# Performance work log

Hardware: AMD Instinct MI355X
Metric: run time of the kernel (lower is better)

## Reference

```python
import jax, jax.numpy as jnp
import numpy as np

I, H, O, L = 128, 1024, 128, 2

def _linear_init(key, out_f, in_f, bias):
    b = 1.0 / np.sqrt(in_f)
    kw, kb = jax.random.split(key)
    W = jax.random.uniform(kw, (out_f, in_f), jnp.float32, -b, b)
    if bias:
        return W, jax.random.uniform(kb, (out_f,), jnp.float32, -b, b)
    return W, None

def setup_inputs() -> dict:
    key = jax.random.key(0)
    ks = jax.random.split(key, 32)
    inp = {
        'x': jax.random.normal(ks[0], (32, 512, I), jnp.float32),
        'h0': jnp.zeros((32, L, H), jnp.float32),
    }
    ki = 1
    in_dim = I
    for l in range(L):
        Wxz, _ = _linear_init(ks[ki], H, in_dim, False); ki += 1
        Whz, bz = _linear_init(ks[ki], H, H, True); ki += 1
        Wxr, _ = _linear_init(ks[ki], H, in_dim, False); ki += 1
        Whr, br = _linear_init(ks[ki], H, H, True); ki += 1
        Wxg, _ = _linear_init(ks[ki], H, in_dim, False); ki += 1
        Whg, bg = _linear_init(ks[ki], H, H, True); ki += 1
        inp.update({f'Wxz{l}': Wxz, f'Whz{l}': Whz, f'bz{l}': bz,
                    f'Wxr{l}': Wxr, f'Whr{l}': Whr, f'br{l}': br,
                    f'Wxg{l}': Wxg, f'Whg{l}': Whg, f'bg{l}': bg})
        in_dim = H
    Wy, by = _linear_init(ks[ki], O, H, True)
    inp['Wy'] = Wy
    inp['by'] = by
    return inp

def _gru_layer(x_seq, h0, Wxz, Whz, bz, Wxr, Whr, br, Wxg, Whg, bg):
    # Precompute all input projections as big GEMMs (B,S,H)
    xz = jnp.einsum('bsi,hi->bsh', x_seq, Wxz)
    xr = jnp.einsum('bsi,hi->bsh', x_seq, Wxr)
    xg = jnp.einsum('bsi,hi->bsh', x_seq, Wxg)
    def step(h, gates):
        gz, gr, gg = gates
        z = jax.nn.sigmoid(gz + h @ Whz.T + bz)
        r = jax.nn.sigmoid(gr + h @ Whr.T + br)
        g = jnp.tanh(gg + (r * h) @ Whg.T + bg)
        h_new = z * h + (1.0 - z) * g
        return h_new, h_new
    # scan over time: (S,B,H)
    hT, hs = jax.lax.scan(step, h0, (xz.transpose(1, 0, 2), xr.transpose(1, 0, 2), xg.transpose(1, 0, 2)))
    return hs.transpose(1, 0, 2), hT

def reference(x, h0,
              Wxz0, Whz0, bz0, Wxr0, Whr0, br0, Wxg0, Whg0, bg0,
              Wxz1, Whz1, bz1, Wxr1, Whr1, br1, Wxg1, Whg1, bg1,
              Wy, by):
    layers = [
        (Wxz0, Whz0, bz0, Wxr0, Whr0, br0, Wxg0, Whg0, bg0),
        (Wxz1, Whz1, bz1, Wxr1, Whr1, br1, Wxg1, Whg1, bg1),
    ]
    seq = x
    finals = []
    for l, p in enumerate(layers):
        seq, hT = _gru_layer(seq, h0[:, l, :], *p)
        finals.append(hT)
    y = jnp.einsum('bsh,oh->bso', seq, Wy) + by  # (B,S,O)
    hidden = jnp.stack(finals, axis=1)  # (B,L,H)
    return y, hidden
```

## Files before the change

### kernel.cpp

```cpp
#include <hip/hip_runtime.h>

typedef unsigned short u16;
typedef unsigned int u32;
typedef unsigned long long u64;
typedef __bf16 bf16x8 __attribute__((ext_vector_type(8)));
typedef float f32x4 __attribute__((ext_vector_type(4)));

union FU { f32x4 f; bf16x8 h; };

__device__ __forceinline__ u16 f2b(float f) {
  unsigned u = __float_as_uint(f);
  return (u16)((u + 0x7fffu + ((u >> 16) & 1u)) >> 16);
}

__device__ __forceinline__ void st_b16_llc(u16* p, u16 v) {
  __hip_atomic_store(p, v, __ATOMIC_RELAXED, __HIP_MEMORY_SCOPE_AGENT);
}

__device__ __forceinline__ u32 ld_dword_cc(const u32* p) {
  u32 v;
  asm volatile("global_load_dword %0, %1, off sc0 sc1\n\ts_waitcnt vmcnt(0)"
               : "=v"(v) : "v"(p) : "memory");
  return v;
}

#define ISSUE8CC(D, P)                                                       \
  asm volatile(                                                              \
      "global_load_dwordx4 %0, %8, off sc0 sc1\n\t"                          \
      "global_load_dwordx4 %1, %8, off offset:64 sc0 sc1\n\t"                \
      "global_load_dwordx4 %2, %8, off offset:128 sc0 sc1\n\t"               \
      "global_load_dwordx4 %3, %8, off offset:192 sc0 sc1\n\t"               \
      "global_load_dwordx4 %4, %8, off offset:256 sc0 sc1\n\t"               \
      "global_load_dwordx4 %5, %8, off offset:320 sc0 sc1\n\t"               \
      "global_load_dwordx4 %6, %8, off offset:384 sc0 sc1\n\t"               \
      "global_load_dwordx4 %7, %8, off offset:448 sc0 sc1"                   \
      : "=&v"((D)[0].f), "=&v"((D)[1].f), "=&v"((D)[2].f), "=&v"((D)[3].f),  \
        "=&v"((D)[4].f), "=&v"((D)[5].f), "=&v"((D)[6].f), "=&v"((D)[7].f)   \
      : "v"(P) : "memory")

#define ISSUE4C(D, P)                                                        \
  asm volatile(                                                              \
      "global_load_dwordx4 %0, %4, off\n\t"                                  \
      "global_load_dwordx4 %1, %4, off offset:64\n\t"                        \
      "global_load_dwordx4 %2, %4, off offset:128\n\t"                       \
      "global_load_dwordx4 %3, %4, off offset:192"                           \
      : "=&v"((D)[0].f), "=&v"((D)[1].f), "=&v"((D)[2].f), "=&v"((D)[3].f)   \
      : "v"(P) : "memory")

#define WAITV(N)                                                             \
  do {                                                                       \
    asm volatile("s_waitcnt vmcnt(" #N ")" ::: "memory");                    \
    __builtin_amdgcn_sched_barrier(0);                                       \
  } while (0)

#define MFMA8ZR(ACC, BUF, KSB)                                               \
  do {                                                                       \
    _Pragma("unroll") for (int j_ = 0; j_ < 8; ++j_)                         \
        ACC = __builtin_amdgcn_mfma_f32_16x16x32_bf16(                       \
            (BUF)[j_].h,                                                     \
            *(const bf16x8*)&zr_frag[(KSB + j_) * 512 + lane * 8],           \
            ACC, 0, 0, 0);                                                   \
  } while (0)
#define MFMA8G(ACC, BUF, KSB)                                                \
  do {                                                                       \
    _Pragma("unroll") for (int j_ = 0; j_ < 8; ++j_)                         \
        ACC = __builtin_amdgcn_mfma_f32_16x16x32_bf16(                       \
            (BUF)[j_].h,                                                     \
            *(const bf16x8*)&g_frag[(KSB + j_) * 256 + boff],                \
            ACC, 0, 0, 0);                                                   \
  } while (0)

__global__ void cast_f32_bf16(const float* __restrict__ in, u16* __restrict__ out, int n) {
  int i = blockIdx.x * 256 + threadIdx.x;
  if (i < n) out[i] = f2b(in[i]);
}

__device__ __forceinline__ void wg_bar(u32* __restrict__ slots, u32 ep,
                                       int bid, int tid, int lane, int w) {
  __syncthreads();
  const int g = bid >> 5;
  u32* gslots = slots + 256;
  if (tid == 0)
    __hip_atomic_store(&slots[g * 32 + (bid & 31)], ep,
                       __ATOMIC_RELAXED, __HIP_MEMORY_SCOPE_AGENT);
  if (w == 0) {
    if ((bid & 31) == 0) {
      const u32* grp = slots + g * 32;
      for (;;) {
        u32 v = ep;
        if (lane < 32) v = ld_dword_cc(&grp[lane]);
        if (__all(v >= ep)) break;
        __builtin_amdgcn_s_sleep(1);
      }
      if (lane == 0)
        __hip_atomic_store(&gslots[g], ep,
                           __ATOMIC_RELAXED, __HIP_MEMORY_SCOPE_AGENT);
    }
    for (;;) {
      u32 v = ld_dword_cc(&gslots[lane & 7]);
      if (__all(v >= ep)) break;
      __builtin_amdgcn_s_sleep(1);
    }
  }
  __syncthreads();
}

__global__ __launch_bounds__(256) void gemm_bt(
    const u16* __restrict__ A, const u16* __restrict__ B,
    int M, int N, int K,
    const float* __restrict__ bias, float* __restrict__ Cf)
{
  __shared__ u16 a_sm[128 * 32];
  __shared__ u16 b_sm[128 * 32];
  const int tid = threadIdx.x;
  const int lane = tid & 63;
  const int wid = tid >> 6;
  const int wm = wid >> 1, wn = wid & 1;
  const int m0 = blockIdx.x * 128, n0 = blockIdx.y * 128;
  const int q = lane >> 4, l15 = lane & 15, l3 = lane & 3;

  f32x4 acc[4][4];
  #pragma unroll
  for (int i = 0; i < 4; ++i)
    #pragma unroll
    for (int j = 0; j < 4; ++j) acc[i][j] = (f32x4){0.f, 0.f, 0.f, 0.f};

  for (int kk = 0; kk < K; kk += 32) {
    __syncthreads();
    #pragma unroll
    for (int p = 0; p < 2; ++p) {
      int idx = p * 256 + tid;
      int r = idx >> 2, cch = idx & 3;
      *(uint4*)&a_sm[r * 32 + ((cch ^ (r & 3)) * 8)] =
          *(const uint4*)&A[(size_t)(m0 + r) * K + kk + cch * 8];
      *(uint4*)&b_sm[r * 32 + ((cch ^ (r & 3)) * 8)] =
          *(const uint4*)&B[(size_t)(n0 + r) * K + kk + cch * 8];
    }
    __syncthreads();
    bf16x8 af[4], bfr[4];
    #pragma unroll
    for (int s = 0; s < 4; ++s) {
      int ra = wm * 64 + s * 16 + l15;
      af[s] = *(const bf16x8*)&a_sm[ra * 32 + ((q ^ l3) * 8)];
      int rb = wn * 64 + s * 16 + l15;
      bfr[s] = *(const bf16x8*)&b_sm[rb * 32 + ((q ^ l3) * 8)];
    }
    #pragma unroll
    for (int si = 0; si < 4; ++si)
      #pragma unroll
      for (int sj = 0; sj < 4; ++sj)
        acc[si][sj] = __builtin_amdgcn_mfma_f32_16x16x32_bf16(af[si], bfr[sj], acc[si][sj], 0, 0, 0);
  }

  #pragma unroll
  for (int si = 0; si < 4; ++si)
    #pragma unroll
    for (int sj = 0; sj < 4; ++sj)
      #pragma unroll
      for (int e = 0; e < 4; ++e) {
        int m = m0 + wm * 64 + si * 16 + q * 4 + e;
        int n = n0 + wn * 64 + sj * 16 + l15;
        Cf[(size_t)m * N + n] = acc[si][sj][e] + (bias ? bias[n] : 0.f);
      }
}

__global__ __launch_bounds__(128, 1) void gru_pipe(
    const u16* __restrict__ Wh0, const u16* __restrict__ Wx0,
    const u16* __restrict__ Wh1, const u16* __restrict__ Wx1,
    const float* __restrict__ bz0, const float* __restrict__ br0, const float* __restrict__ bg0,
    const float* __restrict__ bz1, const float* __restrict__ br1, const float* __restrict__ bg1,
    const u16* __restrict__ xb,
    const float* __restrict__ h0p,
    u16* __restrict__ h0buf,
    u16* __restrict__ hb1,
    u16* __restrict__ rh0b, u16* __restrict__ rh1b,
    u16* __restrict__ seq1,
    float* __restrict__ hid,
    u32* __restrict__ slots)
{
  __shared__ u16 zr_frag[64 * 512];
  __shared__ u16 g_frag[64 * 256];

  const int tid = threadIdx.x;
  const int lane = tid & 63;
  const int w = tid >> 6;
  const int bid = blockIdx.x;
  const bool Lyr1 = bid >= 128;
  const int nb = (bid & 127) * 8;
  const int q = lane >> 4, c15 = lane & 15, nl = c15 & 7;
  const int n_own = nb + nl;
  const bool isz = c15 < 8;
  const int brow = w * 16 + c15;
  const int boff = (q * 8 + nl) * 8;
  const int aoff = brow * 1024 + q * 8;
  const int KS = Lyr1 ? 64 : 36;
  const int IN = Lyr1 ? 1024 : 128;
  const u16* Wh = Lyr1 ? Wh1 : Wh0;
  const u16* Wx = Lyr1 ? Wx1 : Wx0;
  const size_t WXG = (size_t)1024 * IN;

  for (int cidx = tid; cidx < KS * 64; cidx += 128) {
    int ks = cidx >> 6, l = cidx & 63;
    int lq = l >> 4, lc = l & 15;
    int row = nb + (lc & 7), gate = (lc < 8) ? 0 : 1;
    int k0 = ks * 32 + lq * 8;
    const u16* src = (k0 < 1024)
        ? Wh + (size_t)gate * 1048576 + (size_t)row * 1024 + k0
        : Wx + (size_t)gate * WXG + (size_t)row * IN + (k0 - 1024);
    *(uint4*)&zr_frag[cidx * 8] = *(const uint4*)src;
  }
  for (int gidx = tid; gidx < KS * 32; gidx += 128) {
    int ks = gidx >> 5, s = gidx & 31;
    int lq = s >> 3, r8 = s & 7;
    int row = nb + r8, k0 = ks * 32 + lq * 8;
    const u16* src = (k0 < 1024)
        ? Wh + (size_t)2 * 1048576 + (size_t)row * 1024 + k0
        : Wx + (size_t)2 * WXG + (size_t)row * IN + (k0 - 1024);
    *(uint4*)&g_frag[gidx * 8] = *(const uint4*)src;
  }

  const float bias1 = isz ? (Lyr1 ? bz1 : bz0)[n_own] : (Lyr1 ? br1 : br0)[n_own];
  const float bias2 = (Lyr1 ? bg1 : bg0)[n_own];

  float hreg[4], zreg[4] = {0.f, 0.f, 0.f, 0.f};
  #pragma unroll
  for (int e = 0; e < 4; ++e) {
    int b = w * 16 + q * 4 + e;
    float v = h0p[b * 2048 + (Lyr1 ? 1024 : 0) + n_own];
    hreg[e] = v;
    if (isz)
      st_b16_llc((Lyr1 ? hb1 : h0buf + 32768) + b * 1024 + n_own, f2b(v));
  }
  wg_bar(slots, 1, bid, tid, lane, w);

  FU xfu[4];
  FU sA[8], sB[8], sC[8];

  for (int p = 0; p < 1026; ++p) {
    const int t = p >> 1, ph = p & 1;
    if (!Lyr1) {
      if (t < 512) {
        f32x4 a0 = {0.f,0.f,0.f,0.f}, a1 = {0.f,0.f,0.f,0.f};
        if (ph == 0) {
          const u16* hp = h0buf + ((t - 1) & 1) * 32768 + aoff;
          const u16* xp = xb + ((size_t)brow * 512 + t) * 128 + q * 8;
          ISSUE4C(xfu, xp);
          ISSUE8CC(sA, hp);
          ISSUE8CC(sB, hp + 256);
          ISSUE8CC(sC, hp + 512);
          WAITV(16); MFMA8ZR(a0, sA, 0);
          ISSUE8CC(sA, hp + 768);
          WAITV(16); MFMA8ZR(a0, sB, 8);
          WAITV(8);  MFMA8ZR(a0, sC, 16);
          WAITV(0);  MFMA8ZR(a0, sA, 24);
          #pragma unroll
          for (int j = 0; j < 4; ++j)
            a1 = __builtin_amdgcn_mfma_f32_16x16x32_bf16(
                xfu[j].h, *(const bf16x8*)&zr_frag[(32 + j) * 512 + lane * 8], a1, 0, 0, 0);
          float hsh[4];
          #pragma unroll
          for (int e = 0; e < 4; ++e) hsh[e] = __shfl_xor(hreg[e], 8);
          #pragma unroll
          for (int e = 0; e < 4; ++e) {
            float pre = a0[e] + a1[e] + bias1;
            float s = 1.f / (1.f + __expf(-pre));
            if (isz) zreg[e] = s;
            else st_b16_llc(&rh0b[(w * 16 + q * 4 + e) * 1024 + n_own], f2b(s * hsh[e]));
          }
        } else {
          const u16* rp = rh0b + aoff;
          ISSUE8CC(sA, rp);
          ISSUE8CC(sB, rp + 256);
          ISSUE8CC(sC, rp + 512);
          WAITV(16); MFMA8G(a0, sA, 0);
          ISSUE8CC(sA, rp + 768);
          WAITV(16); MFMA8G(a0, sB, 8);
          WAITV(8);  MFMA8G(a0, sC, 16);
          WAITV(0);  MFMA8G(a0, sA, 24);
          #pragma unroll
          for (int j = 0; j < 4; ++j)
            a1 = __builtin_amdgcn_mfma_f32_16x16x32_bf16(
                xfu[j].h, *(const bf16x8*)&g_frag[(32 + j) * 256 + boff], a1, 0, 0, 0);
          if (isz) {
            u16* hout = h0buf + (t & 1) * 32768;
            #pragma unroll
            for (int e = 0; e < 4; ++e) {
              int b = w * 16 + q * 4 + e;
              float pre = a0[e] + a1[e] + bias2;
              float ex = __expf(2.f * pre);
              float gv = 1.f - 2.f / (ex + 1.f);
              float hn = zreg[e] * hreg[e] + (1.f - zreg[e]) * gv;
              hreg[e] = hn;
              st_b16_llc(&hout[b * 1024 + n_own], f2b(hn));
              if (t == 511) hid[b * 2048 + n_own] = hn;
            }
          }
        }
      }
    } else {
      if (t >= 1) {
        const int s = t - 1;
        f32x4 a0 = {0.f,0.f,0.f,0.f}, a1 = {0.f,0.f,0.f,0.f};
        const u16* hp = h0buf + (s & 1) * 32768 + aoff;
        if (ph == 0) {
          const u16* hb = hb1 + aoff;
          ISSUE8CC(sA, hb);
          ISSUE8CC(sB, hb + 256);
          ISSUE8CC(sC, hb + 512);
          WAITV(16); MFMA8ZR(a0, sA, 0);  ISSUE8CC(sA, hb + 768);
          WAITV(16); MFMA8ZR(a0, sB, 8);  ISSUE8CC(sB, hp);
          WAITV(16); MFMA8ZR(a0, sC, 16); ISSUE8CC(sC, hp + 256);
          WAITV(16); MFMA8ZR(a0, sA, 24); ISSUE8CC(sA, hp + 512);
          WAITV(16); MFMA8ZR(a1, sB, 32); ISSUE8CC(sB, hp + 768);
          WAITV(16); MFMA8ZR(a1, sC, 40);
          WAITV(8);  MFMA8ZR(a1, sA, 48);
          WAITV(0);  MFMA8ZR(a1, sB, 56);
          float hsh[4];
          #pragma unroll
          for (int e = 0; e < 4; ++e) hsh[e] = __shfl_xor(hreg[e], 8);
          #pragma unroll
          for (int e = 0; e < 4; ++e) {
            float pre = a0[e] + a1[e] + bias1;
            float sg = 1.f / (1.f + __expf(-pre));
            if (isz) zreg[e] = sg;
            else st_b16_llc(&rh1b[(w * 16 + q * 4 + e) * 1024 + n_own], f2b(sg * hsh[e]));
          }
        } else {
          const u16* rp = rh1b + aoff;
          ISSUE8CC(sA, rp);
          ISSUE8CC(sB, rp + 256);
          ISSUE8CC(sC, rp + 512);
          WAITV(16); MFMA8G(a0, sA, 0);  ISSUE8CC(sA, rp + 768);
          WAITV(16); MFMA8G(a0, sB, 8);  ISSUE8CC(sB, hp);
          WAITV(16); MFMA8G(a0, sC, 16); ISSUE8CC(sC, hp + 256);
          WAITV(16); MFMA8G(a0, sA, 24); ISSUE8CC(sA, hp + 512);
          WAITV(16); MFMA8G(a1, sB, 32); ISSUE8CC(sB, hp + 768);
          WAITV(16); MFMA8G(a1, sC, 40);
          WAITV(8);  MFMA8G(a1, sA, 48);
          WAITV(0);  MFMA8G(a1, sB, 56);
          if (isz) {
            #pragma unroll
            for (int e = 0; e < 4; ++e) {
              int b = w * 16 + q * 4 + e;
              float pre = a0[e] + a1[e] + bias2;
              float ex = __expf(2.f * pre);
              float gv = 1.f - 2.f / (ex + 1.f);
              float hn = zreg[e] * hreg[e] + (1.f - zreg[e]) * gv;
              hreg[e] = hn;
              u16 hnb = f2b(hn);
              st_b16_llc(&hb1[b * 1024 + n_own], hnb);
              seq1[((size_t)b * 512 + s) * 1024 + n_own] = hnb;
              if (s == 511) hid[1024 + b * 2048 + n_own] = hn;
            }
          }
        }
      }
    }
    if (p < 1025) wg_bar(slots, (u32)(p + 2), bid, tid, lane, w);
  }
}

extern "C" void kernel_launch(void* const* d_in, const int* in_sizes, int n_in,
                              void* d_out, int out_size, void* d_ws, size_t ws_size,
                              hipStream_t stream) {
  (void)in_sizes; (void)n_in; (void)out_size; (void)ws_size;
  char* ws = (char*)d_ws;
  const size_t MB = 1024ull * 1024ull;
  u16* seq1 = (u16*)(ws + 0);
  u16* xb   = (u16*)(ws + 32 * MB);
  u16* Wh0  = (u16*)(ws + 36 * MB);
  u16* Wh1  = (u16*)(ws + 42 * MB);
  u16* Wx0  = (u16*)(ws + 48 * MB);
  u16* Wx1  = (u16*)(ws + 49 * MB);
  u16* Wyb  = (u16*)(ws + 55 * MB);
  u16* h0buf = (u16*)(ws + 56 * MB);
  u16* hb1  = (u16*)(ws + 56 * MB + 128 * 1024);
  u16* rh0b = (u16*)(ws + 56 * MB + 192 * 1024);
  u16* rh1b = (u16*)(ws + 56 * MB + 256 * 1024);
  u32* slots = (u32*)(ws + 56 * MB + 320 * 1024);

  hipMemsetAsync(slots, 0, 2048, stream);

  auto cast = [&](const void* in, u16* out, int n) {
    cast_f32_bf16<<<(n + 255) / 256, 256, 0, stream>>>((const float*)in, out, n);
  };
  cast(d_in[0], xb, 2097152);
  cast(d_in[3],  Wh0 + 0,       1048576);
  cast(d_in[6],  Wh0 + 1048576, 1048576);
  cast(d_in[9],  Wh0 + 2097152, 1048576);
  cast(d_in[12], Wh1 + 0,       1048576);
  cast(d_in[15], Wh1 + 1048576, 1048576);
  cast(d_in[18], Wh1 + 2097152, 1048576);
  cast(d_in[2],  Wx0 + 0,      131072);
  cast(d_in[5],  Wx0 + 131072, 131072);
  cast(d_in[8],  Wx0 + 262144, 131072);
  cast(d_in[11], Wx1 + 0,       1048576);
  cast(d_in[14], Wx1 + 1048576, 1048576);
  cast(d_in[17], Wx1 + 2097152, 1048576);
  cast(d_in[20], Wyb, 131072);

  float* y_out = (float*)d_out;
  float* hid = y_out + 2097152;

  gru_pipe<<<256, dim3(128), 0, stream>>>(
      Wh0, Wx0, Wh1, Wx1,
      (const float*)d_in[4],  (const float*)d_in[7],  (const float*)d_in[10],
      (const float*)d_in[13], (const float*)d_in[16], (const float*)d_in[19],
      xb, (const float*)d_in[1],
      h0buf, hb1, rh0b, rh1b, seq1, hid, slots);

  gemm_bt<<<dim3(128, 1), dim3(256), 0, stream>>>(
      seq1, Wyb, 16384, 128, 1024, (const float*)d_in[21], y_out);
}
```

Before: 6.572 ms.

## Replace hierarchical grid barrier with per-wave dependency flags and aggregator wave

Removes the two-level workgroup grid barrier run every pipeline phase. Each compute wave now publishes its own progress counter, and a dedicated third wave in block 0 reduces the counters per dependency group and broadcasts them to replicated flag slots. Each wave waits only on the groups it actually depends on (its own layer, and the other layer with a phase-dependent target) instead of on all blocks. This cuts barrier latency and __syncthreads stalls on the recurrent critical path, at the cost of an extra polling wave, a more fragile ordering protocol, and reliance on the aggregator's polling latency.

```diff
diff --git a/kernel.cpp b/kernel.cpp
--- a/kernel.cpp
+++ b/kernel.cpp
@@ -15,6 +15,10 @@
 
 __device__ __forceinline__ void st_b16_llc(u16* p, u16 v) {
   __hip_atomic_store(p, v, __ATOMIC_RELAXED, __HIP_MEMORY_SCOPE_AGENT);
+}
+
+__device__ __forceinline__ void st_u32_cc(u32* p, u32 v) {
+  asm volatile("global_store_dword %0, %1, off sc0 sc1" :: "v"(p), "v"(v) : "memory");
 }
 
 __device__ __forceinline__ u32 ld_dword_cc(const u32* p) {
@@ -75,36 +79,6 @@
   if (i < n) out[i] = f2b(in[i]);
 }
 
-__device__ __forceinline__ void wg_bar(u32* __restrict__ slots, u32 ep,
-                                       int bid, int tid, int lane, int w) {
-  __syncthreads();
-  const int g = bid >> 5;
-  u32* gslots = slots + 256;
-  if (tid == 0)
-    __hip_atomic_store(&slots[g * 32 + (bid & 31)], ep,
-                       __ATOMIC_RELAXED, __HIP_MEMORY_SCOPE_AGENT);
-  if (w == 0) {
-    if ((bid & 31) == 0) {
-      const u32* grp = slots + g * 32;
-      for (;;) {
-        u32 v = ep;
-        if (lane < 32) v = ld_dword_cc(&grp[lane]);
-        if (__all(v >= ep)) break;
-        __builtin_amdgcn_s_sleep(1);
-      }
-      if (lane == 0)
-        __hip_atomic_store(&gslots[g], ep,
-                           __ATOMIC_RELAXED, __HIP_MEMORY_SCOPE_AGENT);
-    }
-    for (;;) {
-      u32 v = ld_dword_cc(&gslots[lane & 7]);
-      if (__all(v >= ep)) break;
-      __builtin_amdgcn_s_sleep(1);
-    }
-  }
-  __syncthreads();
-}
-
 __global__ __launch_bounds__(256) void gemm_bt(
     const u16* __restrict__ A, const u16* __restrict__ B,
     int M, int N, int K,
@@ -164,7 +138,7 @@
       }
 }
 
-__global__ __launch_bounds__(128, 1) void gru_pipe(
+__global__ __launch_bounds__(192, 1) void gru_pipe(
     const u16* __restrict__ Wh0, const u16* __restrict__ Wx0,
     const u16* __restrict__ Wh1, const u16* __restrict__ Wx1,
     const float* __restrict__ bz0, const float* __restrict__ br0, const float* __restrict__ bg0,
@@ -185,6 +159,8 @@
   const int lane = tid & 63;
   const int w = tid >> 6;
   const int bid = blockIdx.x;
+  u32* lflags = slots + 512;
+
   const bool Lyr1 = bid >= 128;
   const int nb = (bid & 127) * 8;
   const int q = lane >> 4, c15 = lane & 15, nl = c15 & 7;
@@ -199,45 +175,99 @@
   const u16* Wx = Lyr1 ? Wx1 : Wx0;
   const size_t WXG = (size_t)1024 * IN;
 
-  for (int cidx = tid; cidx < KS * 64; cidx += 128) {
-    int ks = cidx >> 6, l = cidx & 63;
-    int lq = l >> 4, lc = l & 15;
-    int row = nb + (lc & 7), gate = (lc < 8) ? 0 : 1;
-    int k0 = ks * 32 + lq * 8;
-    const u16* src = (k0 < 1024)
-        ? Wh + (size_t)gate * 1048576 + (size_t)row * 1024 + k0
-        : Wx + (size_t)gate * WXG + (size_t)row * IN + (k0 - 1024);
-    *(uint4*)&zr_frag[cidx * 8] = *(const uint4*)src;
+  const int d_own = (Lyr1 ? 2 : 0) | (w & 1);
+  const int d_oth = (Lyr1 ? 0 : 2) | (w & 1);
+  u32* slot_ptr = &slots[d_own * 128 + (bid & 127)];
+  const int rrep = bid >> 5;
+  const bool laneOth = (lane & 1) != 0;
+  const u32* lfp = &lflags[rrep * 32 + (laneOth ? d_oth : d_own)];
+
+  float hreg[4], zreg[4] = {0.f, 0.f, 0.f, 0.f};
+
+  if (tid < 128) {
+    for (int cidx = tid; cidx < KS * 64; cidx += 128) {
+      int ks = cidx >> 6, l = cidx & 63;
+      int lq = l >> 4, lc = l & 15;
+      int row = nb + (lc & 7), gate = (lc < 8) ? 0 : 1;
+      int k0 = ks * 32 + lq * 8;
+      const u16* src = (k0 < 1024)
+          ? Wh + (size_t)gate * 1048576 + (size_t)row * 1024 + k0
+          : Wx + (size_t)gate * WXG + (size_t)row * IN + (k0 - 1024);
+      *(uint4*)&zr_frag[cidx * 8] = *(const uint4*)src;
+    }
+    for (int gidx = tid; gidx < KS * 32; gidx += 128) {
+      int ks = gidx >> 5, s = gidx & 31;
+      int lq = s >> 3, r8 = s & 7;
+      int row = nb + r8, k0 = ks * 32 + lq * 8;
+      const u16* src = (k0 < 1024)
+          ? Wh + (size_t)2 * 1048576 + (size_t)row * 1024 + k0
+          : Wx + (size_t)2 * WXG + (size_t)row * IN + (k0 - 1024);
+      *(uint4*)&g_frag[gidx * 8] = *(const uint4*)src;
+    }
+    #pragma unroll
+    for (int e = 0; e < 4; ++e) {
+      int b = w * 16 + q * 4 + e;
+      float v = h0p[b * 2048 + (Lyr1 ? 1024 : 0) + n_own];
+      hreg[e] = v;
+      if (isz)
+        st_b16_llc((Lyr1 ? hb1 : h0buf + 32768) + b * 1024 + n_own, f2b(v));
+    }
   }
-  for (int gidx = tid; gidx < KS * 32; gidx += 128) {
-    int ks = gidx >> 5, s = gidx & 31;
-    int lq = s >> 3, r8 = s & 7;
-    int row = nb + r8, k0 = ks * 32 + lq * 8;
-    const u16* src = (k0 < 1024)
-        ? Wh + (size_t)2 * 1048576 + (size_t)row * 1024 + k0
-        : Wx + (size_t)2 * WXG + (size_t)row * IN + (k0 - 1024);
-    *(uint4*)&g_frag[gidx * 8] = *(const uint4*)src;
+  __syncthreads();
+
+  if (w == 2) {
+    if (bid == 0) {
+      const u32* my = slots + lane * 8;
+      const int dgrp = lane >> 4;
+      u32 pub = 0;
+      for (;;) {
+        uint4 va, vb;
+        asm volatile(
+            "global_load_dwordx4 %0, %2, off sc0 sc1\n\t"
+            "global_load_dwordx4 %1, %2, off offset:16 sc0 sc1\n\t"
+            "s_waitcnt vmcnt(0)"
+            : "=&v"(va), "=&v"(vb) : "v"(my) : "memory");
+        u32 m = min(min(min(va.x, va.y), min(va.z, va.w)),
+                    min(min(vb.x, vb.y), min(vb.z, vb.w)));
+        m = min(m, (u32)__shfl_xor((int)m, 1));
+        m = min(m, (u32)__shfl_xor((int)m, 2));
+        m = min(m, (u32)__shfl_xor((int)m, 4));
+        m = min(m, (u32)__shfl_xor((int)m, 8));
+        if (m > pub) {
+          pub = m;
+          if ((lane & 15) == 0) {
+            #pragma unroll
+            for (int r = 0; r < 8; ++r) st_u32_cc(&lflags[r * 32 + dgrp], m);
+          }
+        }
+        if (__all(pub >= 1026u)) break;
+        __builtin_amdgcn_s_sleep(1);
+      }
+    }
+    return;
   }
+
+  if (lane == 0) st_u32_cc(slot_ptr, 1u);
 
   const float bias1 = isz ? (Lyr1 ? bz1 : bz0)[n_own] : (Lyr1 ? br1 : br0)[n_own];
   const float bias2 = (Lyr1 ? bg1 : bg0)[n_own];
 
-  float hreg[4], zreg[4] = {0.f, 0.f, 0.f, 0.f};
-  #pragma unroll
-  for (int e = 0; e < 4; ++e) {
-    int b = w * 16 + q * 4 + e;
-    float v = h0p[b * 2048 + (Lyr1 ? 1024 : 0) + n_own];
-    hreg[e] = v;
-    if (isz)
-      st_b16_llc((Lyr1 ? hb1 : h0buf + 32768) + b * 1024 + n_own, f2b(v));
-  }
-  wg_bar(slots, 1, bid, tid, lane, w);
-
   FU xfu[4];
   FU sA[8], sB[8], sC[8];
 
   for (int p = 0; p < 1026; ++p) {
     const int t = p >> 1, ph = p & 1;
+
+    {
+      const u32 tgt = laneOth ? ((Lyr1 && ph == 0) ? (u32)(p + 1) : (u32)p)
+                              : (u32)(p + 1);
+      for (;;) {
+        u32 v = ld_dword_cc(lfp);
+        if (__all(v >= tgt)) break;
+        __builtin_amdgcn_s_sleep(1);
+      }
+    }
+
     if (!Lyr1) {
       if (t < 512) {
         f32x4 a0 = {0.f,0.f,0.f,0.f}, a1 = {0.f,0.f,0.f,0.f};
@@ -356,7 +386,11 @@
         }
       }
     }
-    if (p < 1025) wg_bar(slots, (u32)(p + 2), bid, tid, lane, w);
+
+    if (p < 1025) {
+      WAITV(0);
+      if (lane == 0) st_u32_cc(slot_ptr, (u32)(p + 2));
+    }
   }
 }
 
@@ -379,7 +413,7 @@
   u16* rh1b = (u16*)(ws + 56 * MB + 256 * 1024);
   u32* slots = (u32*)(ws + 56 * MB + 320 * 1024);
 
-  hipMemsetAsync(slots, 0, 2048, stream);
+  hipMemsetAsync(slots, 0, 4096, stream);
 
   auto cast = [&](const void* in, u16* out, int n) {
     cast_f32_bf16<<<(n + 255) / 256, 256, 0, stream>>>((const float*)in, out, n);
@@ -402,7 +436,7 @@
   float* y_out = (float*)d_out;
   float* hid = y_out + 2097152;
 
-  gru_pipe<<<256, dim3(128), 0, stream>>>(
+  gru_pipe<<<256, dim3(192), 0, stream>>>(
       Wh0, Wx0, Wh1, Wx1,
       (const float*)d_in[4],  (const float*)d_in[7],  (const float*)d_in[10],
       (const float*)d_in[13], (const float*)d_in[16], (const float*)d_in[19],
```

New measurement: 6.712 ms. +2.1%, slower.
